# Performance work log

Measured on AMD Instinct MI355X. Metric: run time of the kernel, lower is better.

The kernel has to match this reference:

```python
import jax, jax.numpy as jnp
import numpy as np

DILATION = 1  # module init dilation


def _pd_indexing1d(x, d, dilation):
    # x: (B, C, T) float; d: (B, 1, T) float pitch-dependent dilation factors
    B, C, T = x.shape
    dil = jnp.clip((d * dilation).astype(jnp.int32), 1)          # (B,1,T), min 1
    idx = jnp.arange(T, dtype=jnp.int32)[None, None, :]          # (1,1,T)
    idxP = jnp.abs(idx - dil) % T                                # past indices
    idxF0 = idx + dil
    # torch sets overflowed idx to -(idx % T) - 1, i.e. wraps to T - 1 - (idx % T)
    idxF = jnp.where(idxF0 >= T, T - 1 - (idxF0 % T), idxF0)     # future indices
    xP = jnp.take_along_axis(x, jnp.broadcast_to(idxP, x.shape), axis=2)
    xF = jnp.take_along_axis(x, jnp.broadcast_to(idxF, x.shape), axis=2)
    return xP, x, xF


def setup_inputs() -> dict:
    key = jax.random.key(0)
    k1, k2, k3, k4, k5, k6 = jax.random.split(key, 6)
    B, Cin, Cout, T = 8, 512, 512, 8192
    x = jax.random.normal(k1, (B, Cin, T), dtype=jnp.float32)
    d = jax.random.uniform(k2, (B, 1, T), dtype=jnp.float32)
    s = 1.0 / np.sqrt(Cin)
    W0 = jax.random.uniform(k3, (Cout, Cin), jnp.float32, -s, s)  # conv with bias
    b0 = jax.random.uniform(k4, (Cout,), jnp.float32, -s, s)
    W1 = jax.random.uniform(k5, (Cout, Cin), jnp.float32, -s, s)  # no bias
    W2 = jax.random.uniform(k6, (Cout, Cin), jnp.float32, -s, s)  # no bias
    return {"x": x, "d": d, "W0": W0, "b0": b0, "W1": W1, "W2": W2}


def reference(x, d, W0, b0, W1, W2):
    xP, xC, xF = _pd_indexing1d(x, d, DILATION)
    # three 1x1 convs (channel-mixing matmuls), summed; bias only on first conv
    out = jnp.einsum('oc,bct->bot', W0, xP) + b0[None, :, None]
    out = out + jnp.einsum('oc,bct->bot', W1, xC)
    out = out + jnp.einsum('oc,bct->bot', W2, xF)
    return out
```

## Files before the change

### kernel.cpp

```cpp
#include <hip/hip_runtime.h>

#define TT 8192
#define CIN 512
#define COUT 512
#define NB 8
#define KTOT 1536
#define NT 48

typedef __attribute__((ext_vector_type(4))) float f32x4;
typedef __attribute__((ext_vector_type(8))) short bf16x8;

#define GLD16(g, l) __builtin_amdgcn_global_load_lds(                      \
    (const __attribute__((address_space(1))) void*)(g),                    \
    (__attribute__((address_space(3))) void*)(l), 16, 0, 0)

#define CFENCE() asm volatile("" ::: "memory")
#define SBAR() do { CFENCE(); __builtin_amdgcn_s_barrier(); CFENCE(); } while (0)
#define VMCNT0() asm volatile("s_waitcnt vmcnt(0)" ::: "memory")
#define LGKM0() asm volatile("s_waitcnt lgkmcnt(0)" ::: "memory")
#define MFMA(a_, b_, c_) __builtin_amdgcn_mfma_f32_16x16x32_bf16((a_), (b_), (c_), 0, 0, 0)

__device__ inline unsigned short f2bf(float f) {
  union { float f; unsigned int u; } v; v.f = f;
  unsigned int u = v.u;
  unsigned int r = (u + 0x7FFFu + ((u >> 16) & 1u)) >> 16;
  return (unsigned short)r;
}

__global__ void k_convert_w(const float* __restrict__ W0, const float* __restrict__ W1,
                            const float* __restrict__ W2, unsigned short* __restrict__ Wb) {
  int i = blockIdx.x * 256 + threadIdx.x;
  if (i >= COUT * CIN) return;
  const float* Ws = blockIdx.y == 0 ? W0 : (blockIdx.y == 1 ? W1 : W2);
  int o = i >> 9, c = i & 511;
  Wb[(size_t)o * KTOT + blockIdx.y * CIN + c] = f2bf(Ws[i]);
}

__global__ void k_transpose(const float* __restrict__ x, unsigned short* __restrict__ xbT,
                            int b_base) {
  int b = b_base + blockIdx.z;
  const float* xb = x + (size_t)b * CIN * TT;
  unsigned short* xo = xbT + (size_t)blockIdx.z * TT * CIN;
  __shared__ float tile[64][65];
  int t0 = blockIdx.x * 64, c0 = blockIdx.y * 64;
  int tid = threadIdx.x;
#pragma unroll
  for (int it = 0; it < 16; ++it) {
    int L = it * 256 + tid;
    int c = L >> 6, t = L & 63;
    tile[c][t] = xb[(size_t)(c0 + c) * TT + (t0 + t)];
  }
  __syncthreads();
#pragma unroll
  for (int it = 0; it < 16; ++it) {
    int L = it * 256 + tid;
    int t = L >> 6, c = L & 63;
    xo[(size_t)(t0 + t) * CIN + (c0 + c)] = f2bf(tile[c][t]);
  }
}

__global__ __launch_bounds__(512) void k_gemm256(
    const unsigned short* __restrict__ Wb, const unsigned short* __restrict__ xbT,
    const float* __restrict__ d, const float* __restrict__ bias,
    float* __restrict__ out) {
  __shared__ __align__(16) unsigned short As[2][256 * 32];
  __shared__ __align__(16) unsigned short Bs[2][256 * 32];
  const int b = blockIdx.x;
  const int t0 = (blockIdx.y >> 1) * 256;
  const int row0 = (blockIdx.y & 1) * 256;
  const unsigned short* xb = xbT + (size_t)b * TT * CIN;
  const int tid = threadIdx.x;
  const int lane = tid & 63, wid = tid >> 6;
  const int wr = wid >> 2, wc = wid & 3;
  const int l15 = lane & 15, kg = lane >> 4;

  const int srow = tid >> 2;
  const int cSrc8 = ((tid & 3) ^ ((tid >> 3) & 3)) * 8;
  int aOff[2];
  int bOffP[2], bOffC[2], bOffF[2];
#pragma unroll
  for (int j = 0; j < 2; ++j) {
    int r = j * 128 + srow;
    aOff[j] = (row0 + r) * KTOT + cSrc8;
    int t = t0 + r;
    float dv = d[(size_t)b * TT + t];
    int dil = (int)dv; if (dil < 1) dil = 1;
    int p = t - dil; if (p < 0) p = -p; p &= (TT - 1);
    int f0 = t + dil;
    int f = (f0 >= TT) ? (TT - 1 - (f0 & (TT - 1))) : f0;
    bOffP[j] = p * CIN + cSrc8;
    bOffC[j] = t * CIN + cSrc8;
    bOffF[j] = f * CIN + cSrc8;
  }

  const int slot = kg ^ ((l15 >> 1) & 3);
  int aRd[2][4], bRd[4];
#pragma unroll
  for (int mh = 0; mh < 2; ++mh)
#pragma unroll
    for (int mi = 0; mi < 4; ++mi)
      aRd[mh][mi] = (wr * 128 + mh * 64 + mi * 16 + l15) * 32 + slot * 8;
#pragma unroll
  for (int q = 0; q < 4; ++q)
    bRd[q] = (wc * 64 + (q >> 1) * 32 + (q & 1) * 16 + l15) * 32 + slot * 8;

#define STAGE_A(tc_, buf_) do {                                               \
    _Pragma("unroll") for (int j = 0; j < 2; ++j)                             \
      GLD16(Wb + aOff[j] + (tc_) * 32, &As[buf_][j * 4096 + wid * 512]);      \
  } while (0)
#define BSEL(seg_, j_) ((seg_) == 0 ? bOffP[j_] : ((seg_) == 1 ? bOffC[j_] : bOffF[j_]))
#define STAGE_B(tc_, buf_) do {                                               \
    int seg_ = (tc_) >> 4; int k8_ = ((tc_) & 15) * 32;                       \
    _Pragma("unroll") for (int j = 0; j < 2; ++j)                             \
      GLD16(xb + BSEL(seg_, j) + k8_, &Bs[buf_][j * 4096 + wid * 512]);       \
  } while (0)

  STAGE_A(0, 0); STAGE_B(0, 0);
  VMCNT0();
  SBAR();

  bf16x8 af[2][4], bfr[4];
  f32x4 acc[8][4] = {};

#pragma unroll 2
  for (int tc = 0; tc < NT; ++tc) {
    const int cur = tc & 1;
#pragma unroll
    for (int q = 0; q < 4; ++q) bfr[q] = *(const bf16x8*)&Bs[cur][bRd[q]];
#pragma unroll
    for (int mh = 0; mh < 2; ++mh)
#pragma unroll
      for (int mi = 0; mi < 4; ++mi)
        af[mh][mi] = *(const bf16x8*)&As[cur][aRd[mh][mi]];
    if (tc + 1 < NT) { STAGE_A(tc + 1, cur ^ 1); STAGE_B(tc + 1, cur ^ 1); }
    __builtin_amdgcn_s_setprio(1);
#pragma unroll
    for (int mi = 0; mi < 4; ++mi)
#pragma unroll
      for (int q = 0; q < 4; ++q)
        acc[mi][q] = MFMA(af[0][mi], bfr[q], acc[mi][q]);
    __builtin_amdgcn_s_setprio(0);
    __builtin_amdgcn_s_setprio(1);
#pragma unroll
    for (int mi = 0; mi < 4; ++mi)
#pragma unroll
      for (int q = 0; q < 4; ++q)
        acc[4 + mi][q] = MFMA(af[1][mi], bfr[q], acc[4 + mi][q]);
    __builtin_amdgcn_s_setprio(0);
    LGKM0();
    if (tc + 1 < NT) VMCNT0();
    SBAR();
  }

  float* ob = out + (size_t)b * COUT * TT;
#pragma unroll
  for (int mh = 0; mh < 2; ++mh)
#pragma unroll
    for (int mi = 0; mi < 4; ++mi) {
      int m0 = row0 + wr * 128 + mh * 64 + mi * 16 + kg * 4;
#pragma unroll
      for (int q = 0; q < 4; ++q) {
        int t = t0 + wc * 64 + (q >> 1) * 32 + (q & 1) * 16 + l15;
        f32x4 v = acc[mh * 4 + mi][q];
#pragma unroll
        for (int j = 0; j < 4; ++j)
          ob[(size_t)(m0 + j) * TT + t] = v[j] + bias[m0 + j];
      }
    }
}

__global__ __launch_bounds__(256) void k_gemm(
    const unsigned short* __restrict__ Wb, const unsigned short* __restrict__ xbT,
    const float* __restrict__ d, const float* __restrict__ bias,
    float* __restrict__ out, int b_base) {
  __shared__ __align__(16) unsigned short As[128 * 32];
  __shared__ __align__(16) unsigned short Bs[128 * 32];
  int b = b_base + blockIdx.z;
  const unsigned short* xb = xbT + (size_t)blockIdx.z * TT * CIN;
  int row0 = blockIdx.x * 128;
  int t0 = blockIdx.y * 128;
  int tid = threadIdx.x;
  int lane = tid & 63, wid = tid >> 6;
  int wr = wid >> 1, wc = wid & 1;
  int l15 = lane & 15, kg = lane >> 4;
  int rs = tid >> 2, cch = tid & 3;

  const unsigned short* aw[2];
  const unsigned short* bw[2][3];
#pragma unroll
  for (int h = 0; h < 2; ++h) {
    int r = rs + h * 64;
    int cs = cch ^ ((r >> 1) & 3);
    aw[h] = Wb + (size_t)(row0 + r) * KTOT + cs * 8;
    int t = t0 + r;
    float dv = d[(size_t)b * TT + t];
    int dil = (int)dv; if (dil < 1) dil = 1;
    int p = t - dil; if (p < 0) p = -p; p &= (TT - 1);
    int f0 = t + dil;
    int f = (f0 >= TT) ? (TT - 1 - (f0 & (TT - 1))) : f0;
    bw[h][0] = xb + (size_t)p * CIN + cs * 8;
    bw[h][1] = xb + (size_t)t * CIN + cs * 8;
    bw[h][2] = xb + (size_t)f * CIN + cs * 8;
  }
  unsigned short* aDst[2];
  unsigned short* bDst[2];
#pragma unroll
  for (int h = 0; h < 2; ++h) {
    aDst[h] = As + h * 2048 + wid * 512;
    bDst[h] = Bs + h * 2048 + wid * 512;
  }
  int aoff[4], boff[4];
#pragma unroll
  for (int mi = 0; mi < 4; ++mi) {
    int r = wr * 64 + mi * 16 + l15;
    aoff[mi] = r * 32 + (kg ^ ((r >> 1) & 3)) * 8;
  }
#pragma unroll
  for (int ni = 0; ni < 4; ++ni) {
    int r = wc * 64 + ni * 16 + l15;
    boff[ni] = r * 32 + (kg ^ ((r >> 1) & 3)) * 8;
  }
  f32x4 acc[4][4] = {};
#pragma unroll
  for (int s = 0; s < 3; ++s) {
    for (int kt = 0; kt < 16; ++kt) {
      int koff = kt * 32;
#pragma unroll
      for (int h = 0; h < 2; ++h) {
        GLD16(aw[h] + s * CIN + koff, aDst[h]);
        GLD16(bw[h][s] + koff, bDst[h]);
      }
      __syncthreads();
      bf16x8 af[4], bf[4];
#pragma unroll
      for (int mi = 0; mi < 4; ++mi) af[mi] = *(const bf16x8*)(&As[aoff[mi]]);
#pragma unroll
      for (int ni = 0; ni < 4; ++ni) bf[ni] = *(const bf16x8*)(&Bs[boff[ni]]);
#pragma unroll
      for (int mi = 0; mi < 4; ++mi)
#pragma unroll
        for (int ni = 0; ni < 4; ++ni)
          acc[mi][ni] = MFMA(af[mi], bf[ni], acc[mi][ni]);
      __syncthreads();
    }
  }
  float* ob = out + (size_t)b * COUT * TT;
#pragma unroll
  for (int mi = 0; mi < 4; ++mi) {
    int m0 = row0 + wr * 64 + mi * 16 + kg * 4;
#pragma unroll
    for (int ni = 0; ni < 4; ++ni) {
      int t = t0 + wc * 64 + ni * 16 + l15;
#pragma unroll
      for (int j = 0; j < 4; ++j) {
        ob[(size_t)(m0 + j) * TT + t] = acc[mi][ni][j] + bias[m0 + j];
      }
    }
  }
}

extern "C" void kernel_launch(void* const* d_in, const int* in_sizes, int n_in,
                              void* d_out, int out_size, void* d_ws, size_t ws_size,
                              hipStream_t stream) {
  const float* x  = (const float*)d_in[0];
  const float* d  = (const float*)d_in[1];
  const float* W0 = (const float*)d_in[2];
  const float* b0 = (const float*)d_in[3];
  const float* W1 = (const float*)d_in[4];
  const float* W2 = (const float*)d_in[5];
  float* out = (float*)d_out;

  char* ws = (char*)d_ws;
  unsigned short* Wb  = (unsigned short*)ws;
  unsigned short* xbT = (unsigned short*)(ws + (2u << 20));
  const size_t SZ_XBT1 = (size_t)TT * CIN * 2;
  const size_t NEED_FULL = (size_t)(2u << 20) + (size_t)NB * SZ_XBT1;
  const size_t NEED_MIN  = (size_t)(2u << 20) + SZ_XBT1;

  if (ws_size >= NEED_MIN) {
    k_convert_w<<<dim3(1024, 3), 256, 0, stream>>>(W0, W1, W2, Wb);
    if (ws_size >= NEED_FULL) {
      k_transpose<<<dim3(TT / 64, CIN / 64, NB), 256, 0, stream>>>(x, xbT, 0);
      k_gemm256<<<dim3(NB, (TT / 256) * (COUT / 256), 1), 512, 0, stream>>>(
          Wb, xbT, d, b0, out);
    } else {
      for (int b = 0; b < NB; ++b) {
        k_transpose<<<dim3(TT / 64, CIN / 64, 1), 256, 0, stream>>>(x, xbT, b);
        k_gemm<<<dim3(COUT / 128, TT / 128, 1), 256, 0, stream>>>(Wb, xbT, d, b0, out, b);
      }
    }
  } else {
    for (int b = 0; b < NB; ++b) {
      k_transpose<<<dim3(TT / 64, CIN / 64, 1), 256, 0, stream>>>(x, xbT, b);
      k_gemm<<<dim3(COUT / 128, TT / 128, 1), 256, 0, stream>>>(Wb, xbT, d, b0, out, b);
    }
  }
}
```

Measured before the change: 159.7 us.

## Replace 256x256 GEMM tile with 128x256 tile, 256 threads, two blocks per CU

The main GEMM kernel moves from a 256x256 output tile with 512 threads to a 128 (Cout) x 256 (time) tile with 256 threads and launch_bounds(256,2). Each wave now computes a 64x128 sub-tile, and the grid has twice as many blocks. The aim is to let two blocks share a CU so that one block's barrier and load waits overlap with the other's MFMA work. The cost is less reuse of the gathered activation tile: each activation tile is now loaded four times across Cout instead of twice, and register pressure per wave is high.

```diff
diff --git a/kernel.cpp b/kernel.cpp
--- a/kernel.cpp
+++ b/kernel.cpp
@@ -59,30 +59,31 @@
   }
 }
 
-__global__ __launch_bounds__(512) void k_gemm256(
+__global__ __launch_bounds__(256, 2) void k_gemm128(
     const unsigned short* __restrict__ Wb, const unsigned short* __restrict__ xbT,
     const float* __restrict__ d, const float* __restrict__ bias,
     float* __restrict__ out) {
-  __shared__ __align__(16) unsigned short As[2][256 * 32];
+  __shared__ __align__(16) unsigned short As[2][128 * 32];
   __shared__ __align__(16) unsigned short Bs[2][256 * 32];
   const int b = blockIdx.x;
-  const int t0 = (blockIdx.y >> 1) * 256;
-  const int row0 = (blockIdx.y & 1) * 256;
+  const int t0 = (blockIdx.y >> 2) * 256;
+  const int row0 = (blockIdx.y & 3) * 128;
   const unsigned short* xb = xbT + (size_t)b * TT * CIN;
   const int tid = threadIdx.x;
   const int lane = tid & 63, wid = tid >> 6;
-  const int wr = wid >> 2, wc = wid & 3;
+  const int wm = wid >> 1, wn = wid & 1;
   const int l15 = lane & 15, kg = lane >> 4;
 
   const int srow = tid >> 2;
   const int cSrc8 = ((tid & 3) ^ ((tid >> 3) & 3)) * 8;
   int aOff[2];
-  int bOffP[2], bOffC[2], bOffF[2];
-#pragma unroll
-  for (int j = 0; j < 2; ++j) {
-    int r = j * 128 + srow;
-    aOff[j] = (row0 + r) * KTOT + cSrc8;
-    int t = t0 + r;
+  int bOffP[4], bOffC[4], bOffF[4];
+#pragma unroll
+  for (int j = 0; j < 2; ++j)
+    aOff[j] = (row0 + j * 64 + srow) * KTOT + cSrc8;
+#pragma unroll
+  for (int j = 0; j < 4; ++j) {
+    int t = t0 + j * 64 + srow;
     float dv = d[(size_t)b * TT + t];
     int dil = (int)dv; if (dil < 1) dil = 1;
     int p = t - dil; if (p < 0) p = -p; p &= (TT - 1);
@@ -94,58 +95,46 @@
   }
 
   const int slot = kg ^ ((l15 >> 1) & 3);
-  int aRd[2][4], bRd[4];
-#pragma unroll
-  for (int mh = 0; mh < 2; ++mh)
-#pragma unroll
-    for (int mi = 0; mi < 4; ++mi)
-      aRd[mh][mi] = (wr * 128 + mh * 64 + mi * 16 + l15) * 32 + slot * 8;
-#pragma unroll
-  for (int q = 0; q < 4; ++q)
-    bRd[q] = (wc * 64 + (q >> 1) * 32 + (q & 1) * 16 + l15) * 32 + slot * 8;
+  int aRd[4], bRd[8];
+#pragma unroll
+  for (int mi = 0; mi < 4; ++mi)
+    aRd[mi] = (wm * 64 + mi * 16 + l15) * 32 + slot * 8;
+#pragma unroll
+  for (int ni = 0; ni < 8; ++ni)
+    bRd[ni] = (wn * 128 + ni * 16 + l15) * 32 + slot * 8;
 
 #define STAGE_A(tc_, buf_) do {                                               \
     _Pragma("unroll") for (int j = 0; j < 2; ++j)                             \
-      GLD16(Wb + aOff[j] + (tc_) * 32, &As[buf_][j * 4096 + wid * 512]);      \
+      GLD16(Wb + aOff[j] + (tc_) * 32, &As[buf_][j * 2048 + wid * 512]);      \
   } while (0)
 #define BSEL(seg_, j_) ((seg_) == 0 ? bOffP[j_] : ((seg_) == 1 ? bOffC[j_] : bOffF[j_]))
 #define STAGE_B(tc_, buf_) do {                                               \
     int seg_ = (tc_) >> 4; int k8_ = ((tc_) & 15) * 32;                       \
-    _Pragma("unroll") for (int j = 0; j < 2; ++j)                             \
-      GLD16(xb + BSEL(seg_, j) + k8_, &Bs[buf_][j * 4096 + wid * 512]);       \
+    _Pragma("unroll") for (int j = 0; j < 4; ++j)                             \
+      GLD16(xb + BSEL(seg_, j) + k8_, &Bs[buf_][j * 2048 + wid * 512]);       \
   } while (0)
 
   STAGE_A(0, 0); STAGE_B(0, 0);
   VMCNT0();
   SBAR();
 
-  bf16x8 af[2][4], bfr[4];
-  f32x4 acc[8][4] = {};
+  bf16x8 af[4], bf[8];
+  f32x4 acc[4][8] = {};
 
 #pragma unroll 2
   for (int tc = 0; tc < NT; ++tc) {
     const int cur = tc & 1;
 #pragma unroll
-    for (int q = 0; q < 4; ++q) bfr[q] = *(const bf16x8*)&Bs[cur][bRd[q]];
-#pragma unroll
-    for (int mh = 0; mh < 2; ++mh)
-#pragma unroll
-      for (int mi = 0; mi < 4; ++mi)
-        af[mh][mi] = *(const bf16x8*)&As[cur][aRd[mh][mi]];
+    for (int mi = 0; mi < 4; ++mi) af[mi] = *(const bf16x8*)&As[cur][aRd[mi]];
+#pragma unroll
+    for (int ni = 0; ni < 8; ++ni) bf[ni] = *(const bf16x8*)&Bs[cur][bRd[ni]];
     if (tc + 1 < NT) { STAGE_A(tc + 1, cur ^ 1); STAGE_B(tc + 1, cur ^ 1); }
     __builtin_amdgcn_s_setprio(1);
 #pragma unroll
     for (int mi = 0; mi < 4; ++mi)
 #pragma unroll
-      for (int q = 0; q < 4; ++q)
-        acc[mi][q] = MFMA(af[0][mi], bfr[q], acc[mi][q]);
-    __builtin_amdgcn_s_setprio(0);
-    __builtin_amdgcn_s_setprio(1);
-#pragma unroll
-    for (int mi = 0; mi < 4; ++mi)
-#pragma unroll
-      for (int q = 0; q < 4; ++q)
-        acc[4 + mi][q] = MFMA(af[1][mi], bfr[q], acc[4 + mi][q]);
+      for (int ni = 0; ni < 8; ++ni)
+        acc[mi][ni] = MFMA(af[mi], bf[ni], acc[mi][ni]);
     __builtin_amdgcn_s_setprio(0);
     LGKM0();
     if (tc + 1 < NT) VMCNT0();
@@ -154,19 +143,17 @@
 
   float* ob = out + (size_t)b * COUT * TT;
 #pragma unroll
-  for (int mh = 0; mh < 2; ++mh)
-#pragma unroll
-    for (int mi = 0; mi < 4; ++mi) {
-      int m0 = row0 + wr * 128 + mh * 64 + mi * 16 + kg * 4;
-#pragma unroll
-      for (int q = 0; q < 4; ++q) {
-        int t = t0 + wc * 64 + (q >> 1) * 32 + (q & 1) * 16 + l15;
-        f32x4 v = acc[mh * 4 + mi][q];
-#pragma unroll
-        for (int j = 0; j < 4; ++j)
-          ob[(size_t)(m0 + j) * TT + t] = v[j] + bias[m0 + j];
-      }
-    }
+  for (int mi = 0; mi < 4; ++mi) {
+    int m0 = row0 + wm * 64 + mi * 16 + kg * 4;
+#pragma unroll
+    for (int ni = 0; ni < 8; ++ni) {
+      int t = t0 + wn * 128 + ni * 16 + l15;
+      f32x4 v = acc[mi][ni];
+#pragma unroll
+      for (int j = 0; j < 4; ++j)
+        ob[(size_t)(m0 + j) * TT + t] = v[j] + bias[m0 + j];
+    }
+  }
 }
 
 __global__ __launch_bounds__(256) void k_gemm(
@@ -281,7 +268,7 @@
     k_convert_w<<<dim3(1024, 3), 256, 0, stream>>>(W0, W1, W2, Wb);
     if (ws_size >= NEED_FULL) {
       k_transpose<<<dim3(TT / 64, CIN / 64, NB), 256, 0, stream>>>(x, xbT, 0);
-      k_gemm256<<<dim3(NB, (TT / 256) * (COUT / 256), 1), 512, 0, stream>>>(
+      k_gemm128<<<dim3(NB, (TT / 256) * (COUT / 128), 1), 256, 0, stream>>>(
           Wb, xbT, d, b0, out);
     } else {
       for (int b = 0; b < NB; ++b) {
```

Result: no change. 160.4 us (+0.4%).
